# Optimization experiments

Measured on AMD Instinct MI355X. Metric: run time of the kernel, lower is better.

Reference implementation:

```python
import jax, jax.numpy as jnp
import numpy as np

B, N = 2, 512
D_NODE, D_EDGE, D_HID, H = 128, 64, 128, 8
DH = D_HID // H  # per-head dim = 16
SCALE = 1.0 / (D_HID ** 0.5)  # note: scale uses full d_hid as in source


def setup_inputs() -> dict:
    key = jax.random.key(0)
    k1, k2, k3, k4 = jax.random.split(key, 4)
    node_features = jax.random.normal(k1, (B, N, D_NODE), dtype=jnp.float32)
    edge_features = jax.random.normal(k2, (B, N, N, D_EDGE), dtype=jnp.float32)
    mask = jnp.ones((B, N, N), dtype=bool)
    # Linear weights (stored as (in, out); math identical to torch x @ W.T)
    W_node = jax.random.normal(k3, (D_NODE, 3 * D_HID), dtype=jnp.float32) / np.sqrt(D_NODE)
    W_edge = jax.random.normal(k4, (D_EDGE, 3 * D_HID), dtype=jnp.float32) / np.sqrt(D_EDGE)
    return {"node_features": node_features, "edge_features": edge_features,
            "mask": mask, "W_node": W_node, "W_edge": W_edge}


def _split_heads_node(x):
    # (b, n, h*c) -> (b, h, n, c)
    b, n, hc = x.shape
    return x.reshape(b, n, H, hc // H).transpose(0, 2, 1, 3)


def _split_heads_edge(x):
    # (b, n, m, h*c) -> (b, h, n, m, c)
    b, n, m, hc = x.shape
    return x.reshape(b, n, m, H, hc // H).transpose(0, 3, 1, 2, 4)


def reference(node_features, edge_features, mask, W_node, W_edge):
    # node qkv: (b, n, 3*d_hid) -> (b, h, n, 3*dh) -> chunk
    qkv_n = _split_heads_node(node_features @ W_node)
    q_node, k_node, v_node = jnp.split(qkv_n, 3, axis=-1)  # each (b,h,n,dh)
    # edge qkv: (b, n, n, 3*d_hid) -> (b, h, n, n, 3*dh) -> chunk
    qkv_e = _split_heads_edge(edge_features @ W_edge)
    q_edge, k_edge, v_edge = jnp.split(qkv_e, 3, axis=-1)  # each (b,h,n,n,dh)

    q = q_node[:, :, :, None, :] + q_edge   # (b,h,i,j,dh)
    k = k_node[:, :, None, :, :] + k_edge   # (b,h,i,j,dh)
    v = v_node[:, :, None, :, :] + v_edge   # (b,h,i,j,dh)

    dots = SCALE * jnp.einsum('bhijd,bhijd->bhij', q, k)
    attn = jax.nn.softmax(dots, axis=-1)
    out = jnp.einsum('bhij,bhijd->bhid', attn, v)  # (b,h,n,dh)
    # (b,h,n,dh) -> (b,n,h*dh)
    b, h, n, dh = out.shape
    return out.transpose(0, 2, 1, 3).reshape(b, n, h * dh)
```

## Files before the change

kernel.cpp:

```cpp
#include <hip/hip_runtime.h>
#include <hip/hip_bf16.h>

#define NN 512
#define OC 384
#define S2F 0.12751694f

typedef __attribute__((ext_vector_type(8))) short short8;
typedef __attribute__((ext_vector_type(4))) float f32x4;

__device__ __forceinline__ unsigned short f2bf(float x) {
    unsigned u = __builtin_bit_cast(unsigned, x);
    u = (u + 0x7fffu + ((u >> 16) & 1u)) >> 16;
    return (unsigned short)u;
}

__device__ __forceinline__ ushort4 cvt4(f32x4 a) {
    union { ushort4 u4; __hip_bfloat162 h[2]; } r;
    r.h[0] = __float22bfloat162_rn(make_float2(a[0], a[1]));
    r.h[1] = __float22bfloat162_rn(make_float2(a[2], a[3]));
    return r.u4;
}

__global__ __launch_bounds__(256) void prep0_kernel(
    const float* __restrict__ Wn, const float* __restrict__ We,
    const float* __restrict__ node,
    unsigned short* __restrict__ WtN, unsigned short* __restrict__ WtE,
    unsigned short* __restrict__ nodeBf)
{
    int idx = blockIdx.x * 256 + threadIdx.x;
    if (idx < 24576) {
        int o = idx >> 6, k = idx & 63;
        WtE[idx] = f2bf(We[k * OC + o]);
    } else if (idx < 24576 + 49152) {
        int id = idx - 24576;
        int o = id >> 7, k = id & 127;
        WtN[id] = f2bf(Wn[k * OC + o]);
    } else {
        int id = idx - 73728;
        nodeBf[id] = f2bf(node[id]);
    }
}

__global__ __launch_bounds__(256) void prep1_kernel(
    const unsigned short* __restrict__ nodeBf,
    const unsigned short* __restrict__ WtN,
    float* __restrict__ qnF,
    float* __restrict__ nodeKV)
{
    const int t = threadIdx.x;
    const int w = t >> 6;
    const int lane = t & 63;
    const int lj = lane & 15;
    const int quad = lane >> 4;
    const int nbase = blockIdx.x * 32;

    short8 bfr[2][4];
#pragma unroll
    for (int nt = 0; nt < 2; ++nt)
#pragma unroll
        for (int ks = 0; ks < 4; ++ks)
            bfr[nt][ks] = *reinterpret_cast<const short8*>(
                nodeBf + (size_t)(nbase + nt * 16 + lj) * 128 + ks * 32 + quad * 8);

#pragma unroll
    for (int m = 0; m < 6; ++m) {
        int ot = (6 * w + m) * 16;
        short8 afr[4];
#pragma unroll
        for (int ks = 0; ks < 4; ++ks)
            afr[ks] = *reinterpret_cast<const short8*>(
                WtN + (size_t)(ot + lj) * 128 + ks * 32 + quad * 8);
#pragma unroll
        for (int nt = 0; nt < 2; ++nt) {
            f32x4 acc = {0.f, 0.f, 0.f, 0.f};
#pragma unroll
            for (int ks = 0; ks < 4; ++ks)
                acc = __builtin_amdgcn_mfma_f32_16x16x32_bf16(afr[ks], bfr[nt][ks], acc, 0, 0, 0);
            int n = nbase + nt * 16 + lj;
            int bb = n >> 9, ii = n & 511;
#pragma unroll
            for (int r = 0; r < 4; ++r) {
                int o = ot + quad * 4 + r;
                int h = o / 48, rem = o - h * 48;
                size_t base = (size_t)(bb * 8 + h) * NN + ii;
                if (rem < 16) {
                    qnF[base * 16 + rem] = acc[r];
                } else {
                    int d = (rem - 16) & 15;
                    int isv = (rem >= 32) ? 4 : 0;
                    nodeKV[base * 32 + (d >> 2) * 8 + isv + (d & 3)] = acc[r];
                }
            }
        }
    }
}

__global__ __launch_bounds__(512, 4) void rt_attn_main(
    const float* __restrict__ edge,
    const float* __restrict__ qnF,
    const float* __restrict__ nodeKV,
    const unsigned short* __restrict__ WtE,
    float* __restrict__ out)
{
    __shared__ unsigned short sE[2][64 * 72];
    const int bi = blockIdx.x;
    const int b = bi >> 9;
    const int i = bi & 511;
    const int t = threadIdx.x;
    const int h = t >> 6;
    const int lane = t & 63;
    const int lj = lane & 15;
    const int quad = lane >> 4;

    const int sj0 = t >> 4;
    const int sj1 = sj0 + 32;
    const int sc = (t & 15) * 4;

    const float* eBase = edge + (size_t)bi * NN * 64;
    f32x4 pf0, pf1;
    pf0 = *reinterpret_cast<const f32x4*>(eBase + (size_t)sj0 * 64 + sc);
    pf1 = *reinterpret_cast<const f32x4*>(eBase + (size_t)sj1 * 64 + sc);

    short8 afr[3][2];
#pragma unroll
    for (int T = 0; T < 3; ++T)
#pragma unroll
        for (int sec = 0; sec < 2; ++sec)
            afr[T][sec] = *reinterpret_cast<const short8*>(
                WtE + (size_t)(h * 48 + T * 16 + lj) * 64 + sec * 32 + quad * 8);

    const f32x4 qn = *reinterpret_cast<const f32x4*>(
        qnF + ((size_t)(b * 8 + h) * NN + i) * 16 + quad * 4);

    float l = 0.f;
    float oa[4] = {0.f, 0.f, 0.f, 0.f};
    const float* kvBase = nodeKV + (size_t)(b * 8 + h) * NN * 32;

    {
        *reinterpret_cast<ushort4*>(&sE[0][sj0 * 72 + sc]) = cvt4(pf0);
        *reinterpret_cast<ushort4*>(&sE[0][sj1 * 72 + sc]) = cvt4(pf1);
    }
    __syncthreads();

    for (int tt = 0; tt < 8; ++tt) {
        const int cur = tt & 1;
        f32x4 ka[4], va[4];
#pragma unroll
        for (int jn = 0; jn < 4; ++jn) {
            const float* kvp = kvBase + (size_t)(tt * 64 + jn * 16 + lj) * 32 + quad * 8;
            ka[jn] = *reinterpret_cast<const f32x4*>(kvp);
            va[jn] = *reinterpret_cast<const f32x4*>(kvp + 4);
        }
        if (tt < 7) {
            const float* nb = eBase + (size_t)(tt + 1) * 4096;
            pf0 = *reinterpret_cast<const f32x4*>(nb + (size_t)sj0 * 64 + sc);
            pf1 = *reinterpret_cast<const f32x4*>(nb + (size_t)sj1 * 64 + sc);
        }
        float dp[4];
        f32x4 fvv[4];
#pragma unroll
        for (int jn = 0; jn < 4; ++jn) {
            const int jrow = jn * 16 + lj;
            short8 b0 = *reinterpret_cast<const short8*>(&sE[cur][jrow * 72 + quad * 8]);
            short8 b1 = *reinterpret_cast<const short8*>(&sE[cur][jrow * 72 + 32 + quad * 8]);
            f32x4 fq = qn;
            fq = __builtin_amdgcn_mfma_f32_16x16x32_bf16(afr[0][0], b0, fq, 0, 0, 0);
            fq = __builtin_amdgcn_mfma_f32_16x16x32_bf16(afr[0][1], b1, fq, 0, 0, 0);
            f32x4 fk = ka[jn];
            fk = __builtin_amdgcn_mfma_f32_16x16x32_bf16(afr[1][0], b0, fk, 0, 0, 0);
            fk = __builtin_amdgcn_mfma_f32_16x16x32_bf16(afr[1][1], b1, fk, 0, 0, 0);
            f32x4 fv = va[jn];
            fv = __builtin_amdgcn_mfma_f32_16x16x32_bf16(afr[2][0], b0, fv, 0, 0, 0);
            fv = __builtin_amdgcn_mfma_f32_16x16x32_bf16(afr[2][1], b1, fv, 0, 0, 0);
            fvv[jn] = fv;
            float d0 = fq[0] * fk[0];
            d0 = fmaf(fq[1], fk[1], d0);
            d0 = fmaf(fq[2], fk[2], d0);
            d0 = fmaf(fq[3], fk[3], d0);
            dp[jn] = d0;
        }
        float t16[4], t32[4], wg[4];
#pragma unroll
        for (int jn = 0; jn < 4; ++jn) t16[jn] = __shfl_xor(dp[jn], 16);
#pragma unroll
        for (int jn = 0; jn < 4; ++jn) dp[jn] += t16[jn];
#pragma unroll
        for (int jn = 0; jn < 4; ++jn) t32[jn] = __shfl_xor(dp[jn], 32);
#pragma unroll
        for (int jn = 0; jn < 4; ++jn) {
            wg[jn] = exp2f((dp[jn] + t32[jn]) * S2F);
            l += wg[jn];
        }
#pragma unroll
        for (int jn = 0; jn < 4; ++jn)
#pragma unroll
            for (int r = 0; r < 4; ++r)
                oa[r] = fmaf(wg[jn], fvv[jn][r], oa[r]);
        if (tt < 7) {
            *reinterpret_cast<ushort4*>(&sE[cur ^ 1][sj0 * 72 + sc]) = cvt4(pf0);
            *reinterpret_cast<ushort4*>(&sE[cur ^ 1][sj1 * 72 + sc]) = cvt4(pf1);
            __syncthreads();
        }
    }

#pragma unroll
    for (int off = 1; off <= 8; off <<= 1) {
        l += __shfl_xor(l, off);
#pragma unroll
        for (int r = 0; r < 4; ++r) oa[r] += __shfl_xor(oa[r], off);
    }
    if (lj == 0) {
        float inv = 1.0f / l;
        f32x4 o4;
#pragma unroll
        for (int r = 0; r < 4; ++r) o4[r] = oa[r] * inv;
        *reinterpret_cast<f32x4*>(out + (size_t)bi * 128 + h * 16 + quad * 4) = o4;
    }
}

extern "C" void kernel_launch(void* const* d_in, const int* in_sizes, int n_in,
                              void* d_out, int out_size, void* d_ws, size_t ws_size,
                              hipStream_t stream) {
    const float* node = (const float*)d_in[0];
    const float* edge = (const float*)d_in[1];
    const float* Wn = (const float*)d_in[3];
    const float* We = (const float*)d_in[4];
    float* out = (float*)d_out;

    char* ws = (char*)d_ws;
    float* qnF = (float*)ws;
    float* nodeKV = (float*)(ws + 524288);
    unsigned short* WtE = (unsigned short*)(ws + 1572864);
    unsigned short* WtN = (unsigned short*)(ws + 1622016);
    unsigned short* nodeBf = (unsigned short*)(ws + 1720320);

    prep0_kernel<<<800, 256, 0, stream>>>(Wn, We, node, WtN, WtE, nodeBf);
    prep1_kernel<<<32, 256, 0, stream>>>(nodeBf, WtN, qnF, nodeKV);
    rt_attn_main<<<2 * NN, 512, 0, stream>>>(edge, qnF, nodeKV, WtE, out);
}
```

Measured before the change: 241.6 us.

## Stage full edge row into LDS upfront instead of double-buffered tiles

Replaces the per-tile double-buffered prefetch of edge features with a single upfront load of the whole 512-row edge slice into LDS, issued as batches of eight loads per thread, followed by one barrier. This removes the seven per-tile barriers and puts many more memory requests in flight at once. In exchange, LDS use per block grows to about 72KB and the occupancy hint in launch bounds is dropped, so fewer blocks fit per CU. Compute can no longer overlap with the edge loads inside a block.

```diff
diff --git a/kernel.cpp b/kernel.cpp
--- a/kernel.cpp
+++ b/kernel.cpp
@@ -95,14 +95,14 @@
     }
 }
 
-__global__ __launch_bounds__(512, 4) void rt_attn_main(
+__global__ __launch_bounds__(512) void rt_attn_main(
     const float* __restrict__ edge,
     const float* __restrict__ qnF,
     const float* __restrict__ nodeKV,
     const unsigned short* __restrict__ WtE,
     float* __restrict__ out)
 {
-    __shared__ unsigned short sE[2][64 * 72];
+    __shared__ unsigned short sE[512 * 72];
     const int bi = blockIdx.x;
     const int b = bi >> 9;
     const int i = bi & 511;
@@ -112,14 +112,24 @@
     const int lj = lane & 15;
     const int quad = lane >> 4;
 
-    const int sj0 = t >> 4;
-    const int sj1 = sj0 + 32;
-    const int sc = (t & 15) * 4;
-
     const float* eBase = edge + (size_t)bi * NN * 64;
-    f32x4 pf0, pf1;
-    pf0 = *reinterpret_cast<const f32x4*>(eBase + (size_t)sj0 * 64 + sc);
-    pf1 = *reinterpret_cast<const f32x4*>(eBase + (size_t)sj1 * 64 + sc);
+
+    const int j0 = t >> 4;
+    const int c = (t & 15) * 4;
+#pragma unroll
+    for (int half = 0; half < 2; ++half) {
+        f32x4 pf[8];
+#pragma unroll
+        for (int u = 0; u < 8; ++u) {
+            int j = j0 + 32 * (half * 8 + u);
+            pf[u] = *reinterpret_cast<const f32x4*>(eBase + (size_t)j * 64 + c);
+        }
+#pragma unroll
+        for (int u = 0; u < 8; ++u) {
+            int j = j0 + 32 * (half * 8 + u);
+            *reinterpret_cast<ushort4*>(&sE[j * 72 + c]) = cvt4(pf[u]);
+        }
+    }
 
     short8 afr[3][2];
 #pragma unroll
@@ -128,22 +138,16 @@
         for (int sec = 0; sec < 2; ++sec)
             afr[T][sec] = *reinterpret_cast<const short8*>(
                 WtE + (size_t)(h * 48 + T * 16 + lj) * 64 + sec * 32 + quad * 8);
-
     const f32x4 qn = *reinterpret_cast<const f32x4*>(
         qnF + ((size_t)(b * 8 + h) * NN + i) * 16 + quad * 4);
+
+    __syncthreads();
 
     float l = 0.f;
     float oa[4] = {0.f, 0.f, 0.f, 0.f};
     const float* kvBase = nodeKV + (size_t)(b * 8 + h) * NN * 32;
 
-    {
-        *reinterpret_cast<ushort4*>(&sE[0][sj0 * 72 + sc]) = cvt4(pf0);
-        *reinterpret_cast<ushort4*>(&sE[0][sj1 * 72 + sc]) = cvt4(pf1);
-    }
-    __syncthreads();
-
     for (int tt = 0; tt < 8; ++tt) {
-        const int cur = tt & 1;
         f32x4 ka[4], va[4];
 #pragma unroll
         for (int jn = 0; jn < 4; ++jn) {
@@ -151,18 +155,13 @@
             ka[jn] = *reinterpret_cast<const f32x4*>(kvp);
             va[jn] = *reinterpret_cast<const f32x4*>(kvp + 4);
         }
-        if (tt < 7) {
-            const float* nb = eBase + (size_t)(tt + 1) * 4096;
-            pf0 = *reinterpret_cast<const f32x4*>(nb + (size_t)sj0 * 64 + sc);
-            pf1 = *reinterpret_cast<const f32x4*>(nb + (size_t)sj1 * 64 + sc);
-        }
         float dp[4];
         f32x4 fvv[4];
 #pragma unroll
         for (int jn = 0; jn < 4; ++jn) {
-            const int jrow = jn * 16 + lj;
-            short8 b0 = *reinterpret_cast<const short8*>(&sE[cur][jrow * 72 + quad * 8]);
-            short8 b1 = *reinterpret_cast<const short8*>(&sE[cur][jrow * 72 + 32 + quad * 8]);
+            const int jrow = tt * 64 + jn * 16 + lj;
+            short8 b0 = *reinterpret_cast<const short8*>(&sE[jrow * 72 + quad * 8]);
+            short8 b1 = *reinterpret_cast<const short8*>(&sE[jrow * 72 + 32 + quad * 8]);
             f32x4 fq = qn;
             fq = __builtin_amdgcn_mfma_f32_16x16x32_bf16(afr[0][0], b0, fq, 0, 0, 0);
             fq = __builtin_amdgcn_mfma_f32_16x16x32_bf16(afr[0][1], b1, fq, 0, 0, 0);
@@ -196,11 +195,6 @@
 #pragma unroll
             for (int r = 0; r < 4; ++r)
                 oa[r] = fmaf(wg[jn], fvv[jn][r], oa[r]);
-        if (tt < 7) {
-            *reinterpret_cast<ushort4*>(&sE[cur ^ 1][sj0 * 72 + sc]) = cvt4(pf0);
-            *reinterpret_cast<ushort4*>(&sE[cur ^ 1][sj1 * 72 + sc]) = cvt4(pf1);
-            __syncthreads();
-        }
     }
 
 #pragma unroll
```

Measured after the change: 257.1 us. +6.4%, slower.
